# Performance work log

Hardware: AMD Instinct MI355X
Metric: run time of the kernel (lower is better)

The kernel has to match this reference:

```python
import jax, jax.numpy as jnp
import numpy as np

D_MODEL = 512
NHEAD = 8
SEQ = 2048
BATCH = 4


def setup_inputs() -> dict:
    key = jax.random.key(0)
    ks = jax.random.split(key, 6)
    s = 0.02
    return {
        "x": jax.random.normal(ks[0], (SEQ, BATCH, D_MODEL), jnp.float32),
        "w_in_g": jax.random.normal(ks[1], (3 * D_MODEL, D_MODEL), jnp.float32) * s,
        "b_in_g": jnp.zeros((3 * D_MODEL,), jnp.float32),
        "w_out_g": jax.random.normal(ks[2], (D_MODEL, D_MODEL), jnp.float32) * s,
        "b_out_g": jnp.zeros((D_MODEL,), jnp.float32),
        "w_in_l": jax.random.normal(ks[3], (3 * D_MODEL, D_MODEL), jnp.float32) * s,
        "b_in_l": jnp.zeros((3 * D_MODEL,), jnp.float32),
        "w_out_l": jax.random.normal(ks[4], (D_MODEL, D_MODEL), jnp.float32) * s,
        "b_out_l": jnp.zeros((D_MODEL,), jnp.float32),
        "local_window_size": 128,
    }


def _mha(x, w_in, b_in, w_out, b_out, nhead):
    # x: (S, B, D); faithful to torch nn.MultiheadAttention (batch_first=False)
    S, B, D = x.shape
    dh = D // nhead
    qkv = x @ w_in.T + b_in                       # (S, B, 3D)
    q, k, v = jnp.split(qkv, 3, axis=-1)
    q = q.reshape(S, B, nhead, dh)
    k = k.reshape(S, B, nhead, dh)
    v = v.reshape(S, B, nhead, dh)
    scores = jnp.einsum("sbhd,tbhd->bhst", q, k) / jnp.sqrt(jnp.float32(dh))
    attn = jax.nn.softmax(scores, axis=-1)        # (B, H, S, S)
    out = jnp.einsum("bhst,tbhd->sbhd", attn, v).reshape(S, B, D)
    return out @ w_out.T + b_out


def reference(x, w_in_g, b_in_g, w_out_g, b_out_g,
              w_in_l, b_in_l, w_out_l, b_out_l, local_window_size):
    S, B, D = x.shape
    W = int(local_window_size)
    global_out = _mha(x, w_in_g, b_in_g, w_out_g, b_out_g, NHEAD)
    # Non-overlapping local windows tile the sequence (S % W == 0 here),
    # so the per-window loop == window-batched attention.
    nW = S // W
    xw = x.reshape(nW, W, B, D).transpose(1, 0, 2, 3).reshape(W, nW * B, D)
    lw = _mha(xw, w_in_l, b_in_l, w_out_l, b_out_l, NHEAD)
    local_out = lw.reshape(W, nW, B, D).transpose(1, 0, 2, 3).reshape(S, B, D)
    return global_out + local_out
```

## Files before the change

kernel.cpp:

```cpp
#include <hip/hip_runtime.h>
#include <hip/hip_bf16.h>
#include <stdint.h>

typedef __attribute__((ext_vector_type(8))) short bf16x8;
typedef __attribute__((ext_vector_type(4))) float f32x4;

#define DEV __device__ __forceinline__

DEV f32x4 mfma16(bf16x8 a, bf16x8 b, f32x4 c) {
  return __builtin_amdgcn_mfma_f32_16x16x32_bf16(a, b, c, 0, 0, 0);
}

DEV void gload_lds16(const void* g, void* l) {
  __builtin_amdgcn_global_load_lds(
      (__attribute__((address_space(1))) void*)(g),
      (__attribute__((address_space(3))) void*)(l), 16, 0, 0);
}

DEV unsigned short f2bf(float f) {
  __hip_bfloat16 h = __float2bfloat16(f);
  return __builtin_bit_cast(unsigned short, h);
}

__global__ __launch_bounds__(256) void convert_all(
    const float4* __restrict__ s0, const float4* __restrict__ s1,
    const float4* __restrict__ s2, const float4* __restrict__ s3,
    const float4* __restrict__ s4, ushort4* __restrict__ dst)
{
  const int n0 = 1048576, n1 = 196608, n3 = 65536;
  int i = blockIdx.x * 256 + threadIdx.x;
  const float4* s; int off;
  if (i < n0)                 { s = s0; off = 0; }
  else if (i < n0 + n1)       { s = s1; off = n0; }
  else if (i < n0 + 2*n1)     { s = s2; off = n0 + n1; }
  else if (i < n0 + 2*n1+n3)  { s = s3; off = n0 + 2*n1; }
  else                        { s = s4; off = n0 + 2*n1 + n3; }
  float4 v = s[i - off];
  ushort4 o;
  o.x = f2bf(v.x); o.y = f2bf(v.y); o.z = f2bf(v.z); o.w = f2bf(v.w);
  dst[i] = o;
}

#define GEMM_STAGE(Ap, Wp, k0v, bufi)                                          \
  {                                                                            \
    _Pragma("unroll")                                                          \
    for (int is = 0; is < 2; ++is) {                                           \
      const int row = is*64 + (t >> 3);                                        \
      const int slot = (t & 7) ^ (row & 7);                                    \
      gload_lds16((Ap) + (long)(m0 + row)*K + (k0v) + slot*8,                  \
                  (char*)&As[bufi][0] + (is*512 + t)*16);                      \
      gload_lds16((Wp) + (long)(n0 + row)*K + (k0v) + slot*8,                  \
                  (char*)&Ws[bufi][0] + (is*512 + t)*16);                      \
    }                                                                          \
  }

#define GEMM_COMPUTE(cur)                                                      \
  {                                                                            \
    const char* Apl = (const char*)&As[cur][0];                                \
    const char* Wpl = (const char*)&Ws[cur][0];                                \
    __builtin_amdgcn_s_setprio(1);                                             \
    _Pragma("unroll")                                                          \
    for (int kk = 0; kk < 2; ++kk) {                                           \
      bf16x8 af[4], wf[2];                                                     \
      _Pragma("unroll")                                                        \
      for (int i = 0; i < 4; ++i) {                                            \
        const int row = wr*64 + i*16 + l16;                                    \
        const int slot = (kk*4 + g16) ^ (row & 7);                             \
        af[i] = *(const bf16x8*)(Apl + row*128 + slot*16);                     \
      }                                                                        \
      _Pragma("unroll")                                                        \
      for (int j = 0; j < 2; ++j) {                                            \
        const int row = wc*32 + j*16 + l16;                                    \
        const int slot = (kk*4 + g16) ^ (row & 7);                             \
        wf[j] = *(const bf16x8*)(Wpl + row*128 + slot*16);                     \
      }                                                                        \
      _Pragma("unroll")                                                        \
      for (int i = 0; i < 4; ++i)                                              \
        _Pragma("unroll")                                                      \
        for (int j = 0; j < 2; ++j)                                            \
          acc[i][j] = mfma16(af[i], wf[j], acc[i][j]);                         \
    }                                                                          \
    __builtin_amdgcn_s_setprio(0);                                             \
  }

__global__ __launch_bounds__(512) void gemm_qkv(
    const __hip_bfloat16* __restrict__ A0, const __hip_bfloat16* __restrict__ W0,
    const float* __restrict__ b0,
    __hip_bfloat16* __restrict__ qkp, __hip_bfloat16* __restrict__ vtp,
    int M, int N, int K)
{
  __shared__ __attribute__((aligned(16))) __hip_bfloat16 As[2][128*64];
  __shared__ __attribute__((aligned(16))) __hip_bfloat16 Ws[2][128*64];
  const int t = threadIdx.x;
  const int lane = t & 63, wid = t >> 6;
  const int g16 = lane >> 4, l16 = lane & 15;
  const int wr = wid >> 2, wc = wid & 3;
  const int lid = blockIdx.x + (blockIdx.y << 6);
  const int xcd = lid & 7, pos = lid >> 3;
  const int m0 = (xcd*8 + (pos & 7)) * 128, n0 = (pos >> 3) * 128;

  f32x4 acc[4][2] = {};
  const int nks = K >> 6;

  GEMM_STAGE(A0, W0, 0, 0)
  for (int step = 0; step < nks; ++step) {
    const int cur = step & 1;
    if (step + 1 < nks) {
      GEMM_STAGE(A0, W0, (step+1) << 6, cur ^ 1)
      asm volatile("s_waitcnt vmcnt(4)" ::: "memory");
    } else {
      asm volatile("s_waitcnt vmcnt(0)" ::: "memory");
    }
    __builtin_amdgcn_s_barrier();
    asm volatile("" ::: "memory");
    GEMM_COMPUTE(cur)
    asm volatile("" ::: "memory");
    __builtin_amdgcn_s_barrier();
  }

#pragma unroll
  for (int i = 0; i < 4; ++i) {
    const int gr = m0 + wr*64 + i*16 + g16*4;
#pragma unroll
    for (int j = 0; j < 2; ++j) {
      const int gc = n0 + wc*32 + j*16 + l16;
      const float bias = b0[gc];
      if (gc < 1024) {
#pragma unroll
        for (int r = 0; r < 4; ++r)
          qkp[(long)(gr + r)*1024 + gc] = __float2bfloat16(acc[i][j][r] + bias);
      } else {
#pragma unroll
        for (int r = 0; r < 4; ++r) {
          const int m = gr + r;
          vtp[(long)((m & 3)*512 + gc - 1024)*2048 + (m >> 2)] =
              __float2bfloat16(acc[i][j][r] + bias);
        }
      }
    }
  }
}

__global__ __launch_bounds__(512) void gemm_out(
    const __hip_bfloat16* __restrict__ A0, const __hip_bfloat16* __restrict__ W0,
    const float* __restrict__ b0,
    const __hip_bfloat16* __restrict__ A1, const __hip_bfloat16* __restrict__ W1,
    const float* __restrict__ b1,
    float* __restrict__ Cout, int M, int N, int K)
{
  __shared__ __attribute__((aligned(16))) __hip_bfloat16 As[2][128*64];
  __shared__ __attribute__((aligned(16))) __hip_bfloat16 Ws[2][128*64];
  const int t = threadIdx.x;
  const int lane = t & 63, wid = t >> 6;
  const int g16 = lane >> 4, l16 = lane & 15;
  const int wr = wid >> 2, wc = wid & 3;
  const int lid = blockIdx.x + (blockIdx.y << 6);
  const int xcd = lid & 7, pos = lid >> 3;
  const int m0 = (xcd*8 + (pos & 7)) * 128, n0 = (pos >> 3) * 128;

  f32x4 acc[4][2] = {};
  const int nks = K >> 6;
  const int NS = 2*nks;

  GEMM_STAGE(A0, W0, 0, 0)
  for (int step = 0; step < NS; ++step) {
    const int cur = step & 1;
    if (step + 1 < NS) {
      const int nstep = step + 1;
      const __hip_bfloat16* Ap = (nstep >= nks) ? A1 : A0;
      const __hip_bfloat16* Wp = (nstep >= nks) ? W1 : W0;
      const int k0 = ((nstep >= nks) ? (nstep - nks) : nstep) << 6;
      GEMM_STAGE(Ap, Wp, k0, cur ^ 1)
      asm volatile("s_waitcnt vmcnt(4)" ::: "memory");
    } else {
      asm volatile("s_waitcnt vmcnt(0)" ::: "memory");
    }
    __builtin_amdgcn_s_barrier();
    asm volatile("" ::: "memory");
    GEMM_COMPUTE(cur)
    asm volatile("" ::: "memory");
    __builtin_amdgcn_s_barrier();
  }

#pragma unroll
  for (int i = 0; i < 4; ++i) {
    const int gr = m0 + wr*64 + i*16 + g16*4;
#pragma unroll
    for (int j = 0; j < 2; ++j) {
      const int gc = n0 + wc*32 + j*16 + l16;
      const float bias = b0[gc] + b1[gc];
#pragma unroll
      for (int r = 0; r < 4; ++r)
        Cout[(long)(gr + r)*N + gc] = acc[i][j][r] + bias;
    }
  }
}

__global__ __launch_bounds__(512) void flash_all(
    const __hip_bfloat16* __restrict__ qkg, const __hip_bfloat16* __restrict__ vtg,
    __hip_bfloat16* __restrict__ outg,
    const __hip_bfloat16* __restrict__ qkl, const __hip_bfloat16* __restrict__ vtl,
    __hip_bfloat16* __restrict__ outl,
    const int* __restrict__ wptr, int S, int B, int blkoff)
{
  const int t = threadIdx.x, lane = t & 63, w = t >> 6;
  const int g16 = lane >> 4, l16 = lane & 15;
  const int gid = blockIdx.x + blkoff;
  const int isl = gid >= 512;
  const int id = gid & 511;
  const __hip_bfloat16* qk = isl ? qkl : qkg;
  const __hip_bfloat16* vt = isl ? vtl : vtg;
  __hip_bfloat16* outb = isl ? outl : outg;
  const int Wn = isl ? wptr[0] : S;
  const int xcd = id & 7, seq = id >> 3;
  const int bh = xcd + 8*(seq & 3);
  const int qt = seq >> 2;
  const int b = bh >> 3, h = bh & 7;
  const int q0 = qt * 128;
  const int kv0 = (q0 / Wn) * Wn;
  const int nkt = Wn >> 6;
  const int vtb = bh * 64;

  __shared__ __attribute__((aligned(16))) __hip_bfloat16 Kb[2][64*64];
  __shared__ __attribute__((aligned(16))) __hip_bfloat16 Vb[2][64*64];
  __shared__ __attribute__((aligned(16))) short Pl[8][16*72];

  const int qrow = q0 + w*16 + l16;
  bf16x8 qa[2];
  {
    const __hip_bfloat16* qp = qk + ((long)qrow*B + b)*1024 + h*64 + g16*8;
    qa[0] = *(const bf16x8*)(const void*)qp;
    qa[1] = *(const bf16x8*)(const void*)(qp + 32);
  }
  bf16x8 aones;
#pragma unroll
  for (int e = 0; e < 8; ++e) aones[e] = (short)0x3F80;

  f32x4 o[4] = {};
  f32x4 ol = {};
  const float c2 = 0.125f * 1.44269504088896f;

#define STAGE(tile, bufi)                                                      \
  {                                                                            \
    const int kvs_ = kv0 + (tile)*64;                                          \
    const int row_ = t >> 3;                                                   \
    const int sl_ = (t & 7) ^ (row_ & 7);                                      \
    gload_lds16(qk + ((long)(kvs_+row_)*B + b)*1024 + 512 + h*64 + sl_*8,      \
                (char*)&Kb[bufi][0] + t*16);                                   \
    gload_lds16(vt + (long)(vtb + row_)*2048 + kvs_ + sl_*8,                   \
                (char*)&Vb[bufi][0] + t*16);                                   \
  }

  STAGE(0, 0)

  for (int kt = 0; kt < nkt; ++kt) {
    const int cur = kt & 1;
    if (kt + 1 < nkt) {
      STAGE(kt + 1, cur ^ 1)
      asm volatile("s_waitcnt vmcnt(2)" ::: "memory");
    } else {
      asm volatile("s_waitcnt vmcnt(0)" ::: "memory");
    }
    __builtin_amdgcn_s_barrier();
    asm volatile("" ::: "memory");

    f32x4 s[4] = {};
    const char* Kp = (const char*)&Kb[cur][0];
    __builtin_amdgcn_s_setprio(1);
#pragma unroll
    for (int kk = 0; kk < 2; ++kk)
#pragma unroll
      for (int j = 0; j < 4; ++j) {
        const int row = j*16 + l16;
        const int slot = (kk*4 + g16) ^ (row & 7);
        bf16x8 kf = *(const bf16x8*)(Kp + row*128 + slot*16);
        s[j] = mfma16(kf, qa[kk], s[j]);
      }
    __builtin_amdgcn_s_setprio(0);

    short* Pw = &Pl[w][0];
#pragma unroll
    for (int j = 0; j < 4; ++j) {
      short4 pk4;
      pk4.x = (short)f2bf(__builtin_amdgcn_exp2f(s[j][0]*c2));
      pk4.y = (short)f2bf(__builtin_amdgcn_exp2f(s[j][1]*c2));
      pk4.z = (short)f2bf(__builtin_amdgcn_exp2f(s[j][2]*c2));
      pk4.w = (short)f2bf(__builtin_amdgcn_exp2f(s[j][3]*c2));
      *(short4*)(Pw + l16*72 + j*16 + g16*4) = pk4;
    }

    __builtin_amdgcn_s_setprio(1);
#pragma unroll
    for (int kk = 0; kk < 2; ++kk) {
      bf16x8 pf = *(const bf16x8*)(Pw + l16*72 + kk*32 + g16*8);
      ol = mfma16(aones, pf, ol);
#pragma unroll
      for (int dblk = 0; dblk < 4; ++dblk) {
        const int row = dblk*16 + l16;
        const int slot = (kk*4 + g16) ^ (row & 7);
        bf16x8 vf = *(const bf16x8*)((const char*)&Vb[cur][0] + row*128 + slot*16);
        o[dblk] = mfma16(vf, pf, o[dblk]);
      }
    }
    __builtin_amdgcn_s_setprio(0);

    asm volatile("" ::: "memory");
    __builtin_amdgcn_s_barrier();
  }

  const float inv = 1.f / ol[0];
  const long obase = ((long)qrow*B + b)*512 + h*64;
#pragma unroll
  for (int dblk = 0; dblk < 4; ++dblk) {
    ushort4 pk;
    pk.x = f2bf(o[dblk][0]*inv); pk.y = f2bf(o[dblk][1]*inv);
    pk.z = f2bf(o[dblk][2]*inv); pk.w = f2bf(o[dblk][3]*inv);
    *(ushort4*)(outb + obase + dblk*16 + g16*4) = pk;
  }
}

extern "C" void kernel_launch(void* const* d_in, const int* in_sizes, int n_in,
                              void* d_out, int out_size, void* d_ws, size_t ws_size,
                              hipStream_t stream) {
  const float* x   = (const float*)d_in[0];
  const float* wig = (const float*)d_in[1];
  const float* big = (const float*)d_in[2];
  const float* wog = (const float*)d_in[3];
  const float* bog = (const float*)d_in[4];
  const float* wil = (const float*)d_in[5];
  const float* bil = (const float*)d_in[6];
  const float* wol = (const float*)d_in[7];
  const float* bol = (const float*)d_in[8];
  const int*   wsz = (const int*)d_in[9];

  char* ws = (char*)d_ws;
  __hip_bfloat16* xb    = (__hip_bfloat16*)(ws + 0);
  __hip_bfloat16* wigb  = (__hip_bfloat16*)(ws + 8388608);
  __hip_bfloat16* wilb  = (__hip_bfloat16*)(ws + 9961472);
  __hip_bfloat16* wogb  = (__hip_bfloat16*)(ws + 11534336);
  __hip_bfloat16* wolb  = (__hip_bfloat16*)(ws + 12058624);
  __hip_bfloat16* qkg   = (__hip_bfloat16*)(ws + 12582912);
  __hip_bfloat16* qkl   = (__hip_bfloat16*)(ws + 29360128);
  __hip_bfloat16* vtg   = (__hip_bfloat16*)(ws + 46137344);
  __hip_bfloat16* vtl   = (__hip_bfloat16*)(ws + 54525952);
  __hip_bfloat16* attng = xb;

  const int big_ws = ws_size >= (size_t)71303168;
  __hip_bfloat16* attnl = big_ws ? (__hip_bfloat16*)(ws + 62914560)
                                 : qkg;

  convert_all<<<6144, 256, 0, stream>>>(
      (const float4*)x, (const float4*)wig, (const float4*)wil,
      (const float4*)wog, (const float4*)wol, (ushort4*)ws);

  dim3 gq(64, 12);
  gemm_qkv<<<gq, 512, 0, stream>>>(xb, wigb, big, qkg, vtg, 8192, 1536, 512);
  gemm_qkv<<<gq, 512, 0, stream>>>(xb, wilb, bil, qkl, vtl, 8192, 1536, 512);

  if (big_ws) {
    flash_all<<<1024, 512, 0, stream>>>(qkg, vtg, attng, qkl, vtl, attnl,
                                        wsz, 2048, 4, 0);
  } else {
    flash_all<<<512, 512, 0, stream>>>(qkg, vtg, attng, qkl, vtl, attnl,
                                       wsz, 2048, 4, 0);
    flash_all<<<512, 512, 0, stream>>>(qkg, vtg, attng, qkl, vtl, attnl,
                                       wsz, 2048, 4, 512);
  }

  dim3 go(64, 4);
  gemm_out<<<go, 512, 0, stream>>>(attng, wogb, bog, attnl, wolb, bol,
                                   (float*)d_out, 8192, 512, 512);
}
```

Before: 132.6 us.

## Stage V-transpose epilogue through LDS and fold softmax scale into K

The QKV GEMM epilogue now branches per block. For V tiles it transposes results through shared memory and writes 16-byte vectorized rows to the transposed V buffer, instead of scattered 2-byte strided stores. The attention scale and log2e factor are folded into K when it is written, which removes a multiply per score in the attention inner loop. Pre-scaling K before the bf16 rounding changes the numerics slightly, and the LDS buffer is reused for the transpose after the main loop.

New measurement: 120.3 us. -9.3%, faster.

```diff
diff --git a/kernel.cpp b/kernel.cpp
--- a/kernel.cpp
+++ b/kernel.cpp
@@ -3,6 +3,7 @@
 #include <stdint.h>
 
 typedef __attribute__((ext_vector_type(8))) short bf16x8;
+typedef __attribute__((ext_vector_type(8))) unsigned short u16x8;
 typedef __attribute__((ext_vector_type(4))) float f32x4;
 
 #define DEV __device__ __forceinline__
@@ -89,8 +90,9 @@
     __hip_bfloat16* __restrict__ qkp, __hip_bfloat16* __restrict__ vtp,
     int M, int N, int K)
 {
-  __shared__ __attribute__((aligned(16))) __hip_bfloat16 As[2][128*64];
-  __shared__ __attribute__((aligned(16))) __hip_bfloat16 Ws[2][128*64];
+  __shared__ __attribute__((aligned(16))) char SMEM[65536];
+  __hip_bfloat16 (*As)[8192] = (__hip_bfloat16(*)[8192])SMEM;
+  __hip_bfloat16 (*Ws)[8192] = (__hip_bfloat16(*)[8192])(SMEM + 32768);
   const int t = threadIdx.x;
   const int lane = t & 63, wid = t >> 6;
   const int g16 = lane >> 4, l16 = lane & 15;
@@ -118,25 +120,43 @@
     __builtin_amdgcn_s_barrier();
   }
 
-#pragma unroll
-  for (int i = 0; i < 4; ++i) {
-    const int gr = m0 + wr*64 + i*16 + g16*4;
-#pragma unroll
-    for (int j = 0; j < 2; ++j) {
-      const int gc = n0 + wc*32 + j*16 + l16;
-      const float bias = b0[gc];
-      if (gc < 1024) {
+  if (n0 < 1024) {
+#pragma unroll
+    for (int i = 0; i < 4; ++i) {
+      const int gr = m0 + wr*64 + i*16 + g16*4;
+#pragma unroll
+      for (int j = 0; j < 2; ++j) {
+        const int gc = n0 + wc*32 + j*16 + l16;
+        const float bias = b0[gc];
+        const float scl = (gc >= 512) ? 0.180336880f : 1.0f;
 #pragma unroll
         for (int r = 0; r < 4; ++r)
-          qkp[(long)(gr + r)*1024 + gc] = __float2bfloat16(acc[i][j][r] + bias);
-      } else {
-#pragma unroll
-        for (int r = 0; r < 4; ++r) {
-          const int m = gr + r;
-          vtp[(long)((m & 3)*512 + gc - 1024)*2048 + (m >> 2)] =
-              __float2bfloat16(acc[i][j][r] + bias);
-        }
+          qkp[(long)(gr + r)*1024 + gc] =
+              __float2bfloat16((acc[i][j][r] + bias) * scl);
       }
+    }
+  } else {
+    const int n0l = n0 - 1024;
+    short* T = (short*)SMEM;
+#pragma unroll
+    for (int i = 0; i < 4; ++i) {
+      const int sl = wr*16 + i*4 + g16;
+#pragma unroll
+      for (int j = 0; j < 2; ++j) {
+        const int gcl = wc*32 + j*16 + l16;
+        const float bias = b0[n0 + gcl];
+#pragma unroll
+        for (int r = 0; r < 4; ++r)
+          T[gcl*136 + r*32 + sl] = (short)f2bf(acc[i][j][r] + bias);
+      }
+    }
+    __syncthreads();
+    const int d = t & 127, b4 = t >> 7;
+    __hip_bfloat16* dst = vtp + ((long)(b4*512 + n0l + d))*2048 + (m0 >> 2);
+#pragma unroll
+    for (int k = 0; k < 4; ++k) {
+      u16x8 v = *(const u16x8*)(T + d*136 + b4*32 + k*8);
+      *(u16x8*)(dst + k*8) = v;
     }
   }
 }
@@ -238,7 +258,6 @@
 
   f32x4 o[4] = {};
   f32x4 ol = {};
-  const float c2 = 0.125f * 1.44269504088896f;
 
 #define STAGE(tile, bufi)                                                      \
   {                                                                            \
@@ -282,10 +301,10 @@
 #pragma unroll
     for (int j = 0; j < 4; ++j) {
       short4 pk4;
-      pk4.x = (short)f2bf(__builtin_amdgcn_exp2f(s[j][0]*c2));
-      pk4.y = (short)f2bf(__builtin_amdgcn_exp2f(s[j][1]*c2));
-      pk4.z = (short)f2bf(__builtin_amdgcn_exp2f(s[j][2]*c2));
-      pk4.w = (short)f2bf(__builtin_amdgcn_exp2f(s[j][3]*c2));
+      pk4.x = (short)f2bf(__builtin_amdgcn_exp2f(s[j][0]));
+      pk4.y = (short)f2bf(__builtin_amdgcn_exp2f(s[j][1]));
+      pk4.z = (short)f2bf(__builtin_amdgcn_exp2f(s[j][2]));
+      pk4.w = (short)f2bf(__builtin_amdgcn_exp2f(s[j][3]));
       *(short4*)(Pw + l16*72 + j*16 + g16*4) = pk4;
     }
 
```
